# Optimization experiments

Measured on AMD Instinct MI355X. Metric: run time of the kernel, lower is better.

The kernel has to match this reference:

```python
import jax, jax.numpy as jnp
import numpy as np

C_IN = 8      # MASK_BRANCH.OUT_CHANNELS
CH = 8        # MASK_HEAD.CHANNELS
N_LAYERS = 3
SOI = np.array([64.0, 128.0, 256.0, 512.0, 1024.0], dtype=np.float32)  # sizes_of_interest + [last*2]
W_NUMS = [(C_IN + 2) * CH, CH * CH, CH * CH]
B_NUMS = [CH, CH, CH]
NUM_GEN_PARAMS = sum(W_NUMS) + sum(B_NUMS)  # 232


def setup_inputs() -> dict:
    key = jax.random.key(0)
    k1, k2, k3, k4, k5 = jax.random.split(key, 5)
    N_IMG, H, W, N_INST, STRIDE = 2, 100, 136, 400, 8
    mask_feats = jax.random.normal(k1, (N_IMG, C_IN, H, W), dtype=jnp.float32)
    mask_head_params = jax.random.normal(k2, (N_INST, NUM_GEN_PARAMS), dtype=jnp.float32) * 0.1
    # instance centers in input-image pixel coordinates
    instance_locations = jax.random.uniform(k3, (N_INST, 2), dtype=jnp.float32) * jnp.array(
        [W * STRIDE, H * STRIDE], dtype=jnp.float32)
    im_inds = jax.random.randint(k4, (N_INST,), 0, N_IMG, dtype=jnp.int64 if jax.config.jax_enable_x64 else jnp.int32)
    fpn_levels = jax.random.randint(k5, (N_INST,), 0, 5, dtype=jnp.int64 if jax.config.jax_enable_x64 else jnp.int32)
    return {
        'mask_feats': mask_feats,
        'mask_head_params': mask_head_params,
        'instance_locations': instance_locations,
        'im_inds': im_inds,
        'fpn_levels': fpn_levels,
        'mask_feat_stride': STRIDE,
    }


def _compute_locations(h, w, stride):
    # AdelaiDet compute_locations: pixel centers at stride//2 offset, (H*W, 2) as (x, y)
    shifts_x = jnp.arange(w, dtype=jnp.float32) * stride + stride // 2
    shifts_y = jnp.arange(h, dtype=jnp.float32) * stride + stride // 2
    sy, sx = jnp.meshgrid(shifts_y, shifts_x, indexing='ij')
    return jnp.stack([sx.reshape(-1), sy.reshape(-1)], axis=1)  # (H*W, 2)


def _parse_dynamic_params(params):
    # params: (n_inst, 232) -> per-layer weights (n, CH, c_in) and biases (n, CH)
    n = params.shape[0]
    idx = np.cumsum(W_NUMS + B_NUMS)[:-1]
    splits = jnp.split(params, idx, axis=1)
    ws = splits[:N_LAYERS]
    bs = splits[N_LAYERS:]
    weights = [ws[0].reshape(n, CH, C_IN + 2), ws[1].reshape(n, CH, CH), ws[2].reshape(n, CH, CH)]
    biases = [b.reshape(n, CH) for b in bs]
    return weights, biases


def reference(mask_feats, mask_head_params, instance_locations, im_inds, fpn_levels, mask_feat_stride):
    N, _, H, W = mask_feats.shape
    n_inst = mask_head_params.shape[0]
    locations = _compute_locations(H, W, mask_feat_stride)  # (HW, 2)
    # relative coords: (n, 2, HW), normalized by size-of-interest per fpn level
    rel = (instance_locations[:, None, :] - locations[None, :, :]).transpose(0, 2, 1)
    soi = jnp.asarray(SOI)[fpn_levels]  # (n,)
    rel = rel / soi[:, None, None]
    feats = mask_feats[im_inds].reshape(n_inst, C_IN, H * W)
    x = jnp.concatenate([rel, feats], axis=1)  # (n, C_IN+2, HW)
    weights, biases = _parse_dynamic_params(mask_head_params)
    for w, b in zip(weights, biases):
        # per-instance 1x1 conv == batched tiny GEMM; relu after every layer (incl. last)
        x = jax.nn.relu(jnp.einsum('noi,nip->nop', w, x) + b[:, :, None])
    # boundary_enhancement_module is external -> identity; stride==out_stride -> aligned_bilinear factor 1 (identity)
    return x.reshape(n_inst, CH, H, W)
```

## Files before the change

kernel.cpp:

```cpp
#include <hip/hip_runtime.h>

namespace {

constexpr int CH  = 8;
constexpr int CIN = 8;
constexpr int HH  = 100;
constexpr int WW  = 136;
constexpr int HW  = HH * WW;
constexpr int NP  = 232;
constexpr int VP  = 4;
constexpr int BLK = 256;


__global__ __launch_bounds__(BLK)
void dmh_kernel(const float* __restrict__ feats,
                const float* __restrict__ params,
                const float* __restrict__ ilocs,
                const int*   __restrict__ im_inds,
                const int*   __restrict__ lvls,
                const int*   __restrict__ stride_p,
                float*       __restrict__ out)
{
    const int n   = blockIdx.y;
    const int tid = threadIdx.x;

    __shared__ float sp[NP];
    if (tid < NP) sp[tid] = params[(size_t)n * NP + tid];
    __syncthreads();

    const int p0 = (blockIdx.x * BLK + tid) * VP;
    if (p0 >= HW) return;

    const int   im  = im_inds[n];
    const int   lvl = lvls[n];
    const float soi_tab[5] = {64.f, 128.f, 256.f, 512.f, 1024.f};
    const float inv_soi = 1.0f / soi_tab[lvl];
    const float ix = ilocs[2 * n + 0];
    const float iy = ilocs[2 * n + 1];

    const int   s_i = stride_p[0];
    const float fs  = (s_i >= 1 && s_i <= 65536) ? (float)s_i : __int_as_float(s_i);
    const float fh  = floorf(fs * 0.5f);

    float f[CIN][VP];
    const float* fbase = feats + (size_t)im * CIN * HW + p0;
    #pragma unroll
    for (int c = 0; c < CIN; ++c) {
        const float4 v = *reinterpret_cast<const float4*>(fbase + c * HW);
        f[c][0] = v.x; f[c][1] = v.y; f[c][2] = v.z; f[c][3] = v.w;
    }

    float relx[VP], rely[VP];
    #pragma unroll
    for (int j = 0; j < VP; ++j) {
        const int p = p0 + j;
        const int y = p / WW;
        const int x = p - y * WW;
        relx[j] = (ix - ((float)x * fs + fh)) * inv_soi;
        rely[j] = (iy - ((float)y * fs + fh)) * inv_soi;
    }

    float h1[CH][VP];
    #pragma unroll
    for (int o = 0; o < CH; ++o) {
        const float w0 = sp[o * 10 + 0];
        const float w1 = sp[o * 10 + 1];
        const float b  = sp[208 + o];
        #pragma unroll
        for (int j = 0; j < VP; ++j) {
            float a = fmaf(w0, relx[j], fmaf(w1, rely[j], b));
            #pragma unroll
            for (int c = 0; c < CIN; ++c)
                a = fmaf(sp[o * 10 + 2 + c], f[c][j], a);
            h1[o][j] = fmaxf(a, 0.f);
        }
    }

    float h2[CH][VP];
    #pragma unroll
    for (int o = 0; o < CH; ++o) {
        const float b = sp[216 + o];
        #pragma unroll
        for (int j = 0; j < VP; ++j) {
            float a = b;
            #pragma unroll
            for (int i = 0; i < CH; ++i)
                a = fmaf(sp[80 + o * 8 + i], h1[i][j], a);
            h2[o][j] = fmaxf(a, 0.f);
        }
    }

    float h3[CH][VP];
    #pragma unroll
    for (int o = 0; o < CH; ++o) {
        const float b = sp[224 + o];
        #pragma unroll
        for (int j = 0; j < VP; ++j) {
            float a = b;
            #pragma unroll
            for (int i = 0; i < CH; ++i)
                a = fmaf(sp[144 + o * 8 + i], h2[i][j], a);
            h3[o][j] = fmaxf(a, 0.f);
        }
    }

    float* ob = out + (size_t)n * CH * HW + p0;
    #pragma unroll
    for (int o = 0; o < CH; ++o) {
        float4 v;
        v.x = h3[o][0]; v.y = h3[o][1]; v.z = h3[o][2]; v.w = h3[o][3];
        *reinterpret_cast<float4*>(ob + o * HW) = v;
    }
}

}

extern "C" void kernel_launch(void* const* d_in, const int* in_sizes, int n_in,
                              void* d_out, int out_size, void* d_ws, size_t ws_size,
                              hipStream_t stream) {
    const float* feats  = (const float*)d_in[0];
    const float* params = (const float*)d_in[1];
    const float* ilocs  = (const float*)d_in[2];
    const int*   im     = (const int*)d_in[3];
    const int*   lv     = (const int*)d_in[4];
    const int*   st     = (const int*)d_in[5];
    float*       out    = (float*)d_out;

    const int n_inst = in_sizes[1] / NP;
    dim3 grid((HW + BLK * VP - 1) / (BLK * VP), n_inst);
    dmh_kernel<<<grid, BLK, 0, stream>>>(feats, params, ilocs, im, lv, st, out);
}
```

Before: 36.92 us.

## Process eight pixels per thread and use nontemporal output stores

Doubles the pixels per thread from 4 to 8, which halves the grid and amortizes the per-block parameter load and setup across more work. Weights are hoisted into registers for each output channel. The last layer is fused into the store loop, and results are written with nontemporal stores so the output stream does not pollute the cache. The risks are higher register pressure, less occupancy, and tail waste because HW is not a multiple of 2048.

```diff
diff --git a/kernel.cpp b/kernel.cpp
--- a/kernel.cpp
+++ b/kernel.cpp
@@ -8,8 +8,10 @@
 constexpr int WW  = 136;
 constexpr int HW  = HH * WW;
 constexpr int NP  = 232;
-constexpr int VP  = 4;
+constexpr int VP  = 8;
 constexpr int BLK = 256;
+
+typedef float f32x4 __attribute__((ext_vector_type(4)));
 
 
 __global__ __launch_bounds__(BLK)
@@ -46,8 +48,10 @@
     const float* fbase = feats + (size_t)im * CIN * HW + p0;
     #pragma unroll
     for (int c = 0; c < CIN; ++c) {
-        const float4 v = *reinterpret_cast<const float4*>(fbase + c * HW);
-        f[c][0] = v.x; f[c][1] = v.y; f[c][2] = v.z; f[c][3] = v.w;
+        const f32x4 a = *reinterpret_cast<const f32x4*>(fbase + c * HW);
+        const f32x4 b = *reinterpret_cast<const f32x4*>(fbase + c * HW + 4);
+        f[c][0] = a.x; f[c][1] = a.y; f[c][2] = a.z; f[c][3] = a.w;
+        f[c][4] = b.x; f[c][5] = b.y; f[c][6] = b.z; f[c][7] = b.w;
     }
 
     float relx[VP], rely[VP];
@@ -63,15 +67,18 @@
     float h1[CH][VP];
     #pragma unroll
     for (int o = 0; o < CH; ++o) {
-        const float w0 = sp[o * 10 + 0];
-        const float w1 = sp[o * 10 + 1];
-        const float b  = sp[208 + o];
+        const float wx = sp[o * 10 + 0];
+        const float wy = sp[o * 10 + 1];
+        float wf[CIN];
+        #pragma unroll
+        for (int c = 0; c < CIN; ++c) wf[c] = sp[o * 10 + 2 + c];
+        const float b = sp[208 + o];
         #pragma unroll
         for (int j = 0; j < VP; ++j) {
-            float a = fmaf(w0, relx[j], fmaf(w1, rely[j], b));
+            float a = fmaf(wx, relx[j], fmaf(wy, rely[j], b));
             #pragma unroll
             for (int c = 0; c < CIN; ++c)
-                a = fmaf(sp[o * 10 + 2 + c], f[c][j], a);
+                a = fmaf(wf[c], f[c][j], a);
             h1[o][j] = fmaxf(a, 0.f);
         }
     }
@@ -79,37 +86,41 @@
     float h2[CH][VP];
     #pragma unroll
     for (int o = 0; o < CH; ++o) {
+        float w[CH];
+        #pragma unroll
+        for (int i = 0; i < CH; ++i) w[i] = sp[80 + o * 8 + i];
         const float b = sp[216 + o];
         #pragma unroll
         for (int j = 0; j < VP; ++j) {
             float a = b;
             #pragma unroll
             for (int i = 0; i < CH; ++i)
-                a = fmaf(sp[80 + o * 8 + i], h1[i][j], a);
+                a = fmaf(w[i], h1[i][j], a);
             h2[o][j] = fmaxf(a, 0.f);
-        }
-    }
-
-    float h3[CH][VP];
-    #pragma unroll
-    for (int o = 0; o < CH; ++o) {
-        const float b = sp[224 + o];
-        #pragma unroll
-        for (int j = 0; j < VP; ++j) {
-            float a = b;
-            #pragma unroll
-            for (int i = 0; i < CH; ++i)
-                a = fmaf(sp[144 + o * 8 + i], h2[i][j], a);
-            h3[o][j] = fmaxf(a, 0.f);
         }
     }
 
     float* ob = out + (size_t)n * CH * HW + p0;
     #pragma unroll
     for (int o = 0; o < CH; ++o) {
-        float4 v;
-        v.x = h3[o][0]; v.y = h3[o][1]; v.z = h3[o][2]; v.w = h3[o][3];
-        *reinterpret_cast<float4*>(ob + o * HW) = v;
+        float w[CH];
+        #pragma unroll
+        for (int i = 0; i < CH; ++i) w[i] = sp[144 + o * 8 + i];
+        const float b = sp[224 + o];
+        float r[VP];
+        #pragma unroll
+        for (int j = 0; j < VP; ++j) {
+            float a = b;
+            #pragma unroll
+            for (int i = 0; i < CH; ++i)
+                a = fmaf(w[i], h2[i][j], a);
+            r[j] = fmaxf(a, 0.f);
+        }
+        f32x4 v0, v1;
+        v0.x = r[0]; v0.y = r[1]; v0.z = r[2]; v0.w = r[3];
+        v1.x = r[4]; v1.y = r[5]; v1.z = r[6]; v1.w = r[7];
+        __builtin_nontemporal_store(v0, reinterpret_cast<f32x4*>(ob + o * HW));
+        __builtin_nontemporal_store(v1, reinterpret_cast<f32x4*>(ob + o * HW + 4));
     }
 }
 
```

New measurement: 81.00 us. +119.4%, slower.
